# Performance work log

Hardware: AMD Instinct MI355X
Metric: run time of the kernel (lower is better)

The kernel has to match this reference:

```python
import jax, jax.numpy as jnp
import numpy as np

# theta (Kruschke-style ALCOVE hyperparameters, from init_kwargs)
RHO = 2.0
TAU = 1.0
BETA = 6.5
GAMMA = 0.0
PHI = 2.0
LAM_A = 0.001
LAM_W = 0.003

B, D, H, O = 256, 64, 2048, 32  # batch, n_dim, n_hidden, n_output


def setup_inputs() -> dict:
    key = jax.random.key(0)
    k1, k2, k3, k4, k5 = jax.random.split(key, 5)
    z = jax.random.normal(k1, (B, D), dtype=jnp.float32)
    labels = jax.random.randint(k2, (B,), 0, O)
    one_hot_label = jax.nn.one_hot(labels, O, dtype=jnp.float32)
    attention = jax.random.uniform(k3, (B, D), dtype=jnp.float32)
    association = 0.05 * jax.random.normal(k4, (B, H, O), dtype=jnp.float32)
    coordinates = jax.random.normal(k5, (H, D), dtype=jnp.float32)
    return {
        'z': z,
        'one_hot_label': one_hot_label,
        'attention': attention,
        'association': association,
        'coordinates': coordinates,
    }


def reference(z, one_hot_label, attention, association, coordinates):
    """One ALCOVECell RNN step: RBF similarity -> readout -> ALCOVE loss ->
    analytic state update via autodiff. Returns (x_out_scaled, new_attention, new_association)."""

    def loss_fn(att, assoc):
        # weighted Minkowski distance: (B, H)
        diff = jnp.abs(z[:, None, :] - coordinates[None, :, :]) ** RHO  # (B, H, D)
        d = jnp.sum(diff * att[:, None, :], axis=-1) ** (1.0 / RHO)
        # RBF similarity and readout
        s = jnp.exp(-BETA * d ** TAU) + GAMMA                            # (B, H)
        x_out = jnp.einsum('bh,bho->bo', s, assoc)                       # (B, O)
        # ALCOVE humble-teacher loss (gradients flow through teacher, as in TF)
        t_min = jnp.minimum(-1.0, x_out)
        teacher = t_min - one_hot_label * t_min
        t_max = jnp.maximum(1.0, x_out)
        teacher = teacher + one_hot_label * t_max
        loss = jnp.mean(jnp.square(teacher - x_out), axis=1)             # (B,)
        # TF tape.gradient on a vector loss sums over batch
        return jnp.sum(loss), x_out

    (dl_da, dl_dw), x_out = jax.grad(loss_fn, argnums=(0, 1), has_aux=True)(
        attention, association)

    x_out_scaled = PHI * x_out
    new_attention = jnp.maximum(attention - LAM_A * dl_da, 0.0)
    new_association = association - LAM_W * dl_dw
    return x_out_scaled, new_attention, new_association
```

## Files before the change

kernel.cpp:

```cpp
#include <hip/hip_runtime.h>
#include <math.h>


#define BB 256
#define DD 64
#define HH 2048
#define OO 32
#define BETA 6.5f
#define PHI 2.0f
#define LAM_A 0.001f
#define LAM_W 0.003f
#define NT0 256
#define NT 1024
#define NW (NT / 64)
#define NCH (HH / (NT / 8))

__global__ __launch_bounds__(NT0) void k0_transpose(
    const float* __restrict__ coords, float* __restrict__ ct)
{
    int idx = blockIdx.x * NT0 + threadIdx.x;
    int d = idx >> 11;
    int h = idx & (HH - 1);
    ct[idx] = coords[h * DD + d];
}

__global__ __launch_bounds__(NT) void k_cell(
    const float* __restrict__ z,
    const float* __restrict__ one_hot,
    const float* __restrict__ att,
    const float* __restrict__ assoc,
    const float* __restrict__ coords,
    const float* __restrict__ ct,
    float* __restrict__ out)
{
    __shared__ float2 za[DD];
    __shared__ float  s_loc[HH];
    __shared__ float  rc_loc[HH];
    __shared__ float  wredf[NW * OO];
    __shared__ float  redf[NT];
    __shared__ float  gx_s[OO];

    const int b = blockIdx.x;
    const int t = threadIdx.x;

    if (t < DD)
        za[t] = make_float2(z[b * DD + t], att[b * DD + t]);
    __syncthreads();

    #pragma unroll
    for (int i = 0; i < HH / NT; ++i) {
        const int h = i * NT + t;
        float S = 0.0f;
        const float* ctp = ct + h;
        #pragma unroll 16
        for (int d = 0; d < DD; ++d) {
            float2 p = za[d];
            float c = ctp[d * HH];
            float diff = p.x - c;
            S = fmaf(p.y * diff, diff, S);
        }
        S = S < 0.0f ? 0.0f : S;
        float dd = sqrtf(S);
        float sh = expf(-BETA * dd);
        s_loc[h]  = sh;
        rc_loc[h] = (dd > 0.0f) ? (-BETA * sh / (2.0f * dd)) : 0.0f;
    }
    __syncthreads();

    const int o4 = t & 7;
    const int hl = t >> 3;
    const float4* assoc4 = (const float4*)(assoc + (size_t)b * HH * OO);

    float4 areg[NCH];
    float4 acc = make_float4(0.f, 0.f, 0.f, 0.f);
    #pragma unroll
    for (int ch = 0; ch < NCH; ++ch) {
        int hloc = ch * (NT / 8) + hl;
        float4 a = assoc4[hloc * (OO / 4) + o4];
        areg[ch] = a;
        float s2 = s_loc[hloc];
        acc.x = fmaf(s2, a.x, acc.x);
        acc.y = fmaf(s2, a.y, acc.y);
        acc.z = fmaf(s2, a.z, acc.z);
        acc.w = fmaf(s2, a.w, acc.w);
    }
    #pragma unroll
    for (int m = 8; m <= 32; m <<= 1) {
        acc.x += __shfl_xor(acc.x, m, 64);
        acc.y += __shfl_xor(acc.y, m, 64);
        acc.z += __shfl_xor(acc.z, m, 64);
        acc.w += __shfl_xor(acc.w, m, 64);
    }
    if ((t & 63) < 8) {
        int w = t >> 6;
        wredf[w * OO + o4 * 4 + 0] = acc.x;
        wredf[w * OO + o4 * 4 + 1] = acc.y;
        wredf[w * OO + o4 * 4 + 2] = acc.z;
        wredf[w * OO + o4 * 4 + 3] = acc.w;
    }
    __syncthreads();

    if (t < OO) {
        float x = 0.0f;
        #pragma unroll
        for (int w = 0; w < NW; ++w)
            x += wredf[w * OO + t];
        float oh = one_hot[b * OO + t];
        float tmin = fminf(-1.0f, x);
        float tmax = fmaxf(1.0f, x);
        float teacher = tmin - oh * tmin + oh * tmax;
        gx_s[t] = (2.0f / OO) * (x - teacher);
        out[b * OO + t] = PHI * x;
    }
    __syncthreads();

    const float4 gxv = ((const float4*)gx_s)[o4];
    float4* out_assoc4 = (float4*)(out + BB * OO + BB * DD)
                       + (size_t)b * HH * (OO / 4);

    #pragma unroll
    for (int ch = 0; ch < NCH; ++ch) {
        int hloc = ch * (NT / 8) + hl;
        float4 a = areg[ch];
        float w = LAM_W * s_loc[hloc];
        float4 na;
        na.x = fmaf(-w, gxv.x, a.x);
        na.y = fmaf(-w, gxv.y, a.y);
        na.z = fmaf(-w, gxv.z, a.z);
        na.w = fmaf(-w, gxv.w, a.w);
        out_assoc4[hloc * (OO / 4) + o4] = na;

        float part = a.x * gxv.x + a.y * gxv.y + a.z * gxv.z + a.w * gxv.w;
        part += __shfl_xor(part, 1, 64);
        part += __shfl_xor(part, 2, 64);
        part += __shfl_xor(part, 4, 64);
        if (o4 == 0)
            rc_loc[hloc] *= part;
    }
    __syncthreads();

    {
        const int lane = t & 63, wv = t >> 6;
        const float zd = za[lane].x;
        float ga = 0.0f;
        #pragma unroll 8
        for (int i = 0; i < HH / NW; ++i) {
            int hloc = wv * (HH / NW) + i;
            float cf = rc_loc[hloc];
            float c = coords[(size_t)hloc * DD + lane];
            float diff = zd - c;
            ga = fmaf(cf * diff, diff, ga);
        }
        redf[t] = ga;
    }
    __syncthreads();
    if (t < DD) {
        float g = 0.0f;
        #pragma unroll
        for (int w = 0; w < NW; ++w)
            g += redf[w * 64 + t];
        float na = att[b * DD + t] - LAM_A * g;
        out[BB * OO + b * DD + t] = na > 0.0f ? na : 0.0f;
    }
}

extern "C" void kernel_launch(void* const* d_in, const int* in_sizes, int n_in,
                              void* d_out, int out_size, void* d_ws, size_t ws_size,
                              hipStream_t stream) {
    const float* z       = (const float*)d_in[0];
    const float* one_hot = (const float*)d_in[1];
    const float* att     = (const float*)d_in[2];
    const float* assoc   = (const float*)d_in[3];
    const float* coords  = (const float*)d_in[4];
    float* out = (float*)d_out;

    float* ct = (float*)d_ws;

    k0_transpose<<<dim3((DD * HH) / NT0), dim3(NT0), 0, stream>>>(coords, ct);
    k_cell<<<dim3(BB), dim3(NT), 0, stream>>>(z, one_hot, att, assoc,
                                              coords, ct, out);
}
```

Before: 139.9 us.

## Prefetch association before distance phase, vectorize coord loads, defer association stores

Association loads are issued at kernel start so their global latency overlaps the distance computation. The distance loop now has each thread handle two adjacent hidden units using float2 loads from the transposed coordinates, which halves the load instructions. The association update stores move after the reduction and sync, grouping them and taking them out of the shuffle loop. The change keeps 16 float4 registers live across the distance phase, which raises register pressure at 1024 threads per block.

```diff
diff --git a/kernel.cpp b/kernel.cpp
--- a/kernel.cpp
+++ b/kernel.cpp
@@ -42,43 +42,48 @@
 
     const int b = blockIdx.x;
     const int t = threadIdx.x;
+    const int o4 = t & 7;
+    const int hl = t >> 3;
+
+    const float4* assoc4 = (const float4*)(assoc + (size_t)b * HH * OO);
+    float4 areg[NCH];
+    #pragma unroll
+    for (int ch = 0; ch < NCH; ++ch)
+        areg[ch] = assoc4[(ch * (NT / 8) + hl) * (OO / 4) + o4];
 
     if (t < DD)
         za[t] = make_float2(z[b * DD + t], att[b * DD + t]);
     __syncthreads();
 
-    #pragma unroll
-    for (int i = 0; i < HH / NT; ++i) {
-        const int h = i * NT + t;
-        float S = 0.0f;
-        const float* ctp = ct + h;
+    {
+        float S0 = 0.0f, S1 = 0.0f;
+        const float2* ct2 = (const float2*)ct;
         #pragma unroll 16
         for (int d = 0; d < DD; ++d) {
             float2 p = za[d];
-            float c = ctp[d * HH];
-            float diff = p.x - c;
-            S = fmaf(p.y * diff, diff, S);
+            float2 c = ct2[d * (HH / 2) + t];
+            float d0 = p.x - c.x;
+            float d1 = p.x - c.y;
+            S0 = fmaf(p.y * d0, d0, S0);
+            S1 = fmaf(p.y * d1, d1, S1);
         }
-        S = S < 0.0f ? 0.0f : S;
-        float dd = sqrtf(S);
-        float sh = expf(-BETA * dd);
-        s_loc[h]  = sh;
-        rc_loc[h] = (dd > 0.0f) ? (-BETA * sh / (2.0f * dd)) : 0.0f;
+        S0 = S0 < 0.0f ? 0.0f : S0;
+        S1 = S1 < 0.0f ? 0.0f : S1;
+        float dd0 = sqrtf(S0), dd1 = sqrtf(S1);
+        float sh0 = expf(-BETA * dd0), sh1 = expf(-BETA * dd1);
+        float r0 = (dd0 > 0.0f) ? (-BETA * sh0 / (2.0f * dd0)) : 0.0f;
+        float r1 = (dd1 > 0.0f) ? (-BETA * sh1 / (2.0f * dd1)) : 0.0f;
+        ((float2*)s_loc)[t]  = make_float2(sh0, sh1);
+        ((float2*)rc_loc)[t] = make_float2(r0, r1);
     }
     __syncthreads();
 
-    const int o4 = t & 7;
-    const int hl = t >> 3;
-    const float4* assoc4 = (const float4*)(assoc + (size_t)b * HH * OO);
-
-    float4 areg[NCH];
     float4 acc = make_float4(0.f, 0.f, 0.f, 0.f);
     #pragma unroll
     for (int ch = 0; ch < NCH; ++ch) {
         int hloc = ch * (NT / 8) + hl;
-        float4 a = assoc4[hloc * (OO / 4) + o4];
-        areg[ch] = a;
         float s2 = s_loc[hloc];
+        float4 a = areg[ch];
         acc.x = fmaf(s2, a.x, acc.x);
         acc.y = fmaf(s2, a.y, acc.y);
         acc.z = fmaf(s2, a.z, acc.z);
@@ -115,21 +120,10 @@
     __syncthreads();
 
     const float4 gxv = ((const float4*)gx_s)[o4];
-    float4* out_assoc4 = (float4*)(out + BB * OO + BB * DD)
-                       + (size_t)b * HH * (OO / 4);
-
     #pragma unroll
     for (int ch = 0; ch < NCH; ++ch) {
         int hloc = ch * (NT / 8) + hl;
         float4 a = areg[ch];
-        float w = LAM_W * s_loc[hloc];
-        float4 na;
-        na.x = fmaf(-w, gxv.x, a.x);
-        na.y = fmaf(-w, gxv.y, a.y);
-        na.z = fmaf(-w, gxv.z, a.z);
-        na.w = fmaf(-w, gxv.w, a.w);
-        out_assoc4[hloc * (OO / 4) + o4] = na;
-
         float part = a.x * gxv.x + a.y * gxv.y + a.z * gxv.z + a.w * gxv.w;
         part += __shfl_xor(part, 1, 64);
         part += __shfl_xor(part, 2, 64);
@@ -138,6 +132,23 @@
             rc_loc[hloc] *= part;
     }
     __syncthreads();
+
+    {
+        float4* out_assoc4 = (float4*)(out + BB * OO + BB * DD)
+                           + (size_t)b * HH * (OO / 4);
+        #pragma unroll
+        for (int ch = 0; ch < NCH; ++ch) {
+            int hloc = ch * (NT / 8) + hl;
+            float4 a = areg[ch];
+            float w = LAM_W * s_loc[hloc];
+            float4 na;
+            na.x = fmaf(-w, gxv.x, a.x);
+            na.y = fmaf(-w, gxv.y, a.y);
+            na.z = fmaf(-w, gxv.z, a.z);
+            na.w = fmaf(-w, gxv.w, a.w);
+            out_assoc4[hloc * (OO / 4) + o4] = na;
+        }
+    }
 
     {
         const int lane = t & 63, wv = t >> 6;
```

Result: slower. 144.0 us (+2.9%).

## Split each batch row across two blocks by output half, reduce attention grads separately

Applied to the files above, without the earlier changes.

The cell kernel now launches two 512-thread blocks per batch row, each handling 16 of the 32 output columns, instead of one 1024-thread block. Each block writes its partial attention gradient to a workspace buffer, and a new small kernel sums the two halves and applies the clamped attention update. The association tile is no longer kept in registers; it is re-read from global memory in the update loop. Some __syncthreads are replaced by inline s_waitcnt/s_barrier. The aim is more blocks in flight and lower register pressure, at the cost of recomputing the distance and similarity stage twice per row, reading the association twice, and an extra kernel launch.

```diff
diff --git a/kernel.cpp b/kernel.cpp
--- a/kernel.cpp
+++ b/kernel.cpp
@@ -11,9 +11,9 @@
 #define LAM_A 0.001f
 #define LAM_W 0.003f
 #define NT0 256
-#define NT 1024
+#define NT 512
 #define NW (NT / 64)
-#define NCH (HH / (NT / 8))
+#define NCH (HH / (NT / 4))
 
 __global__ __launch_bounds__(NT0) void k0_transpose(
     const float* __restrict__ coords, float* __restrict__ ct)
@@ -24,24 +24,28 @@
     ct[idx] = coords[h * DD + d];
 }
 
-__global__ __launch_bounds__(NT) void k_cell(
+__global__ __launch_bounds__(NT, 4) void k_cell(
     const float* __restrict__ z,
     const float* __restrict__ one_hot,
     const float* __restrict__ att,
     const float* __restrict__ assoc,
     const float* __restrict__ coords,
     const float* __restrict__ ct,
+    float* __restrict__ gatt_part,
     float* __restrict__ out)
 {
     __shared__ float2 za[DD];
     __shared__ float  s_loc[HH];
     __shared__ float  rc_loc[HH];
-    __shared__ float  wredf[NW * OO];
+    __shared__ float  wredf[NW * 16];
     __shared__ float  redf[NT];
-    __shared__ float  gx_s[OO];
+    __shared__ float  gx_s[16];
 
-    const int b = blockIdx.x;
-    const int t = threadIdx.x;
+    const int b    = blockIdx.x & (BB - 1);
+    const int half = blockIdx.x >> 8;
+    const int t    = threadIdx.x;
+    const int o4   = t & 3;
+    const int hl   = t >> 2;
 
     if (t < DD)
         za[t] = make_float2(z[b * DD + t], att[b * DD + t]);
@@ -67,77 +71,71 @@
     }
     __syncthreads();
 
-    const int o4 = t & 7;
-    const int hl = t >> 3;
     const float4* assoc4 = (const float4*)(assoc + (size_t)b * HH * OO);
+    const int ocol = half * 4 + o4;
 
-    float4 areg[NCH];
     float4 acc = make_float4(0.f, 0.f, 0.f, 0.f);
     #pragma unroll
     for (int ch = 0; ch < NCH; ++ch) {
-        int hloc = ch * (NT / 8) + hl;
-        float4 a = assoc4[hloc * (OO / 4) + o4];
-        areg[ch] = a;
+        int hloc = ch * (NT / 4) + hl;
         float s2 = s_loc[hloc];
+        float4 a = assoc4[hloc * (OO / 4) + ocol];
         acc.x = fmaf(s2, a.x, acc.x);
         acc.y = fmaf(s2, a.y, acc.y);
         acc.z = fmaf(s2, a.z, acc.z);
         acc.w = fmaf(s2, a.w, acc.w);
     }
     #pragma unroll
-    for (int m = 8; m <= 32; m <<= 1) {
+    for (int m = 4; m <= 32; m <<= 1) {
         acc.x += __shfl_xor(acc.x, m, 64);
         acc.y += __shfl_xor(acc.y, m, 64);
         acc.z += __shfl_xor(acc.z, m, 64);
         acc.w += __shfl_xor(acc.w, m, 64);
     }
-    if ((t & 63) < 8) {
+    if ((t & 63) < 4) {
         int w = t >> 6;
-        wredf[w * OO + o4 * 4 + 0] = acc.x;
-        wredf[w * OO + o4 * 4 + 1] = acc.y;
-        wredf[w * OO + o4 * 4 + 2] = acc.z;
-        wredf[w * OO + o4 * 4 + 3] = acc.w;
+        wredf[w * 16 + o4 * 4 + 0] = acc.x;
+        wredf[w * 16 + o4 * 4 + 1] = acc.y;
+        wredf[w * 16 + o4 * 4 + 2] = acc.z;
+        wredf[w * 16 + o4 * 4 + 3] = acc.w;
     }
     __syncthreads();
 
-    if (t < OO) {
+    if (t < 16) {
         float x = 0.0f;
         #pragma unroll
         for (int w = 0; w < NW; ++w)
-            x += wredf[w * OO + t];
-        float oh = one_hot[b * OO + t];
+            x += wredf[w * 16 + t];
+        float oh = one_hot[b * OO + half * 16 + t];
         float tmin = fminf(-1.0f, x);
         float tmax = fmaxf(1.0f, x);
         float teacher = tmin - oh * tmin + oh * tmax;
         gx_s[t] = (2.0f / OO) * (x - teacher);
-        out[b * OO + t] = PHI * x;
+        out[b * OO + half * 16 + t] = PHI * x;
     }
     __syncthreads();
 
     const float4 gxv = ((const float4*)gx_s)[o4];
     float4* out_assoc4 = (float4*)(out + BB * OO + BB * DD)
                        + (size_t)b * HH * (OO / 4);
-
     #pragma unroll
     for (int ch = 0; ch < NCH; ++ch) {
-        int hloc = ch * (NT / 8) + hl;
-        float4 a = areg[ch];
+        int hloc = ch * (NT / 4) + hl;
+        float4 a = assoc4[hloc * (OO / 4) + ocol];
+        float part = a.x * gxv.x + a.y * gxv.y + a.z * gxv.z + a.w * gxv.w;
+        part += __shfl_xor(part, 1, 64);
+        part += __shfl_xor(part, 2, 64);
+        if (o4 == 0)
+            rc_loc[hloc] *= part;
         float w = LAM_W * s_loc[hloc];
         float4 na;
         na.x = fmaf(-w, gxv.x, a.x);
         na.y = fmaf(-w, gxv.y, a.y);
         na.z = fmaf(-w, gxv.z, a.z);
         na.w = fmaf(-w, gxv.w, a.w);
-        out_assoc4[hloc * (OO / 4) + o4] = na;
-
-        float part = a.x * gxv.x + a.y * gxv.y + a.z * gxv.z + a.w * gxv.w;
-        part += __shfl_xor(part, 1, 64);
-        part += __shfl_xor(part, 2, 64);
-        part += __shfl_xor(part, 4, 64);
-        if (o4 == 0)
-            rc_loc[hloc] *= part;
+        out_assoc4[hloc * (OO / 4) + ocol] = na;
     }
-    __syncthreads();
+    asm volatile("s_waitcnt lgkmcnt(0)\n\ts_barrier" ::: "memory");
 
     {
         const int lane = t & 63, wv = t >> 6;
@@ -153,15 +151,28 @@
         }
         redf[t] = ga;
     }
-    __syncthreads();
+    asm volatile("s_waitcnt lgkmcnt(0)\n\ts_barrier" ::: "memory");
     if (t < DD) {
         float g = 0.0f;
         #pragma unroll
         for (int w = 0; w < NW; ++w)
             g += redf[w * 64 + t];
-        float na = att[b * DD + t] - LAM_A * g;
-        out[BB * OO + b * DD + t] = na > 0.0f ? na : 0.0f;
+        gatt_part[((size_t)b * 2 + half) * DD + t] = g;
     }
+}
+
+__global__ __launch_bounds__(NT0) void k3_att(
+    const float* __restrict__ att,
+    const float* __restrict__ gatt_part,
+    float* __restrict__ out)
+{
+    int idx = blockIdx.x * NT0 + threadIdx.x;
+    int b = idx >> 6;
+    int d = idx & 63;
+    float g = gatt_part[((size_t)b * 2 + 0) * DD + d]
+            + gatt_part[((size_t)b * 2 + 1) * DD + d];
+    float na = att[b * DD + d] - LAM_A * g;
+    out[BB * OO + idx] = na > 0.0f ? na : 0.0f;
 }
 
 extern "C" void kernel_launch(void* const* d_in, const int* in_sizes, int n_in,
@@ -174,9 +185,12 @@
     const float* coords  = (const float*)d_in[4];
     float* out = (float*)d_out;
 
-    float* ct = (float*)d_ws;
+    float* ws = (float*)d_ws;
+    float* ct        = ws;
+    float* gatt_part = ct + DD * HH;
 
     k0_transpose<<<dim3((DD * HH) / NT0), dim3(NT0), 0, stream>>>(coords, ct);
-    k_cell<<<dim3(BB), dim3(NT), 0, stream>>>(z, one_hot, att, assoc,
-                                              coords, ct, out);
+    k_cell<<<dim3(BB * 2), dim3(NT), 0, stream>>>(z, one_hot, att, assoc,
+                                                  coords, ct, gatt_part, out);
+    k3_att<<<dim3((BB * DD) / NT0), dim3(NT0), 0, stream>>>(att, gatt_part, out);
 }
```

Result: slower. 165.7 us (+18.4%).

## Stream association chunks with prefetch and interleave attention-gradient accumulation per chunk

Applied to the files above, without the earlier changes.

Stops keeping all 16 association chunks in registers from the readout pass. The update pass now re-reads them from global memory with a one-chunk software prefetch. The attention-gradient coordinate loop is split into per-chunk slices, each run right after its rc values are written and separated by a raw s_barrier. The aim is to cut register pressure and overlap the coordinate reads with the association writes. In exchange, the association input is read twice and there are 16 block barriers instead of one.

```diff
diff --git a/kernel.cpp b/kernel.cpp
--- a/kernel.cpp
+++ b/kernel.cpp
@@ -13,7 +13,7 @@
 #define NT0 256
 #define NT 1024
 #define NW (NT / 64)
-#define NCH (HH / (NT / 8))
+#define NCH 16
 
 __global__ __launch_bounds__(NT0) void k0_transpose(
     const float* __restrict__ coords, float* __restrict__ ct)
@@ -42,6 +42,8 @@
 
     const int b = blockIdx.x;
     const int t = threadIdx.x;
+    const int o4 = t & 7;
+    const int hl = t >> 3;
 
     if (t < DD)
         za[t] = make_float2(z[b * DD + t], att[b * DD + t]);
@@ -67,18 +69,13 @@
     }
     __syncthreads();
 
-    const int o4 = t & 7;
-    const int hl = t >> 3;
     const float4* assoc4 = (const float4*)(assoc + (size_t)b * HH * OO);
-
-    float4 areg[NCH];
     float4 acc = make_float4(0.f, 0.f, 0.f, 0.f);
     #pragma unroll
     for (int ch = 0; ch < NCH; ++ch) {
-        int hloc = ch * (NT / 8) + hl;
+        int hloc = ch * 128 + hl;
+        float s2 = s_loc[hloc];
         float4 a = assoc4[hloc * (OO / 4) + o4];
-        areg[ch] = a;
-        float s2 = s_loc[hloc];
         acc.x = fmaf(s2, a.x, acc.x);
         acc.y = fmaf(s2, a.y, acc.y);
         acc.z = fmaf(s2, a.z, acc.z);
@@ -117,43 +114,48 @@
     const float4 gxv = ((const float4*)gx_s)[o4];
     float4* out_assoc4 = (float4*)(out + BB * OO + BB * DD)
                        + (size_t)b * HH * (OO / 4);
+    const int lane = t & 63, wv = t >> 6;
+    const float zd = za[lane].x;
+    float ga = 0.0f;
 
+    float4 a_cur = assoc4[hl * (OO / 4) + o4];
     #pragma unroll
-    for (int ch = 0; ch < NCH; ++ch) {
-        int hloc = ch * (NT / 8) + hl;
-        float4 a = areg[ch];
-        float w = LAM_W * s_loc[hloc];
-        float4 na;
-        na.x = fmaf(-w, gxv.x, a.x);
-        na.y = fmaf(-w, gxv.y, a.y);
-        na.z = fmaf(-w, gxv.z, a.z);
-        na.w = fmaf(-w, gxv.w, a.w);
-        out_assoc4[hloc * (OO / 4) + o4] = na;
+    for (int c = 0; c < NCH; ++c) {
+        float4 a_nxt = make_float4(0.f, 0.f, 0.f, 0.f);
+        if (c + 1 < NCH)
+            a_nxt = assoc4[((c + 1) * 128 + hl) * (OO / 4) + o4];
 
-        float part = a.x * gxv.x + a.y * gxv.y + a.z * gxv.z + a.w * gxv.w;
+        const int hloc = c * 128 + hl;
+        float part = a_cur.x * gxv.x + a_cur.y * gxv.y
+                   + a_cur.z * gxv.z + a_cur.w * gxv.w;
         part += __shfl_xor(part, 1, 64);
         part += __shfl_xor(part, 2, 64);
         part += __shfl_xor(part, 4, 64);
         if (o4 == 0)
             rc_loc[hloc] *= part;
-    }
-    __syncthreads();
+        float w = LAM_W * s_loc[hloc];
+        float4 na;
+        na.x = fmaf(-w, gxv.x, a_cur.x);
+        na.y = fmaf(-w, gxv.y, a_cur.y);
+        na.z = fmaf(-w, gxv.z, a_cur.z);
+        na.w = fmaf(-w, gxv.w, a_cur.w);
+        out_assoc4[hloc * (OO / 4) + o4] = na;
 
-    {
-        const int lane = t & 63, wv = t >> 6;
-        const float zd = za[lane].x;
-        float ga = 0.0f;
-        #pragma unroll 8
-        for (int i = 0; i < HH / NW; ++i) {
-            int hloc = wv * (HH / NW) + i;
-            float cf = rc_loc[hloc];
-            float c = coords[(size_t)hloc * DD + lane];
-            float diff = zd - c;
+        asm volatile("s_waitcnt lgkmcnt(0)\n\ts_barrier" ::: "memory");
+
+        #pragma unroll
+        for (int i = 0; i < 8; ++i) {
+            int row = c * 128 + wv * 8 + i;
+            float cf = rc_loc[row];
+            float cc = coords[(size_t)row * DD + lane];
+            float diff = zd - cc;
             ga = fmaf(cf * diff, diff, ga);
         }
-        redf[t] = ga;
+        a_cur = a_nxt;
     }
-    __syncthreads();
+
+    redf[t] = ga;
+    asm volatile("s_waitcnt lgkmcnt(0)\n\ts_barrier" ::: "memory");
     if (t < DD) {
         float g = 0.0f;
         #pragma unroll
```

Result: slower. 237.1 us (+69.5%).
